# Kernel tuning notes

Measured on AMD Instinct MI355X. Metric: run time of the kernel, lower is better.

Reference implementation:

```python
import jax, jax.numpy as jnp
import numpy as np
from itertools import permutations

EPS = 1e-14


def setup_inputs() -> dict:
    key = jax.random.key(0)
    k1, k2 = jax.random.split(key)
    B, T, S = 512, 8000, 3
    pred = jax.random.normal(k1, (B, T, S), dtype=jnp.float32)
    targets = (jax.random.uniform(k2, (B, T, S)) < 0.3).astype(jnp.float32)
    mask = jnp.ones((B, T), dtype=jnp.float32)
    return {"pred_frames_out": pred, "targets": targets, "mask": mask}


def _pit_loss(pred, targets, mask):
    # pred, targets: [B, T, S]; mask: [B, T]
    B, T, S = pred.shape
    x = pred[:, :, :, None]        # [B,T,S_pred,1]
    t = targets[:, :, None, :]     # [B,T,1,S_tgt]
    # numerically stable BCE-with-logits (same as nn.BCEWithLogitsLoss)
    bce = jnp.maximum(x, 0.0) - x * t + jnp.log1p(jnp.exp(-jnp.abs(x)))  # [B,T,S,S]
    msum = jnp.sum(mask, axis=1) + EPS                                    # [B]
    # cost[b,i,j] = masked mean over time of BCE(pred_i, target_j)
    cost = jnp.einsum('btij,bt->bij', bce, mask) / msum[:, None, None]    # [B,S,S]
    perms = jnp.asarray(list(permutations(range(S))), dtype=jnp.int32)    # [P,S]
    idx_i = jnp.arange(S)[None, :]                                        # [1,S]
    # perm_loss[b,p] = mean_i cost[b, i, perms[p,i]]
    perm_loss = jnp.mean(cost[:, idx_i, perms], axis=-1)                  # [B,P]
    best_val = jnp.min(perm_loss, axis=1)                                 # [B]
    best_idx = jnp.argmin(perm_loss, axis=1)                              # [B]
    return best_val.mean(), best_idx


def reference(pred_frames_out, targets, mask):
    return _pit_loss(pred_frames_out, targets, mask)
```

## Files before the change

### kernel.cpp

```cpp
#include <hip/hip_runtime.h>
#include <math.h>

#define BB 512
#define TT 8000
#define SS 3
#define CH 4
#define TC (TT/CH)
#define NV (TC/4)
#define NACC 13

__device__ __forceinline__ double waveReduceD(double v) {
    #pragma unroll
    for (int o = 32; o > 0; o >>= 1) v += __shfl_down(v, o, 64);
    return v;
}

__global__ __launch_bounds__(256) void pit_partial(
        const float* __restrict__ pred,
        const float* __restrict__ tgt,
        const float* __restrict__ mask,
        double* __restrict__ partials) {
    int blk = blockIdx.x;
    int b = blk / CH, c = blk % CH;
    int tbase = c * TC;
    const float* pp = pred + ((size_t)b * TT + tbase) * 3;
    const float* tp = tgt  + ((size_t)b * TT + tbase) * 3;
    const float* mp = mask + (size_t)b * TT + tbase;

    float acc[NACC];
    #pragma unroll
    for (int k = 0; k < NACC; k++) acc[k] = 0.0f;

    for (int item = threadIdx.x; item < NV; item += 256) {
        const float4* p4 = (const float4*)(pp + (size_t)item * 12);
        float4 pa = p4[0], pb = p4[1], pc = p4[2];
        const float4* t4 = (const float4*)(tp + (size_t)item * 12);
        float4 ta = t4[0], tb = t4[1], tc = t4[2];
        float4 mm = *(const float4*)(mp + (size_t)item * 4);

        float px[4][3] = {{pa.x,pa.y,pa.z},{pa.w,pb.x,pb.y},
                          {pb.z,pb.w,pc.x},{pc.y,pc.z,pc.w}};
        float tx[4][3] = {{ta.x,ta.y,ta.z},{ta.w,tb.x,tb.y},
                          {tb.z,tb.w,tc.x},{tc.y,tc.z,tc.w}};
        float mv[4] = {mm.x, mm.y, mm.z, mm.w};

        #pragma unroll
        for (int u = 0; u < 4; u++) {
            float m = mv[u];
            acc[12] += m;
            #pragma unroll
            for (int i = 0; i < 3; i++) {
                float x = px[u][i];
                float sp = fmaxf(x, 0.0f) + __logf(1.0f + __expf(-fabsf(x)));
                acc[i] = fmaf(m, sp, acc[i]);
                float mx = m * x;
                #pragma unroll
                for (int j = 0; j < 3; j++) {
                    acc[3 + i*3 + j] = fmaf(mx, tx[u][j], acc[3 + i*3 + j]);
                }
            }
        }
    }

    __shared__ double sdata[4][NACC];
    int lane = threadIdx.x & 63, wave = threadIdx.x >> 6;
    #pragma unroll
    for (int k = 0; k < NACC; k++) {
        double v = waveReduceD((double)acc[k]);
        if (lane == 0) sdata[wave][k] = v;
    }
    __syncthreads();
    if (threadIdx.x == 0) {
        #pragma unroll
        for (int k = 0; k < NACC; k++) {
            double s = sdata[0][k] + sdata[1][k] + sdata[2][k] + sdata[3][k];
            partials[(size_t)blk * NACC + k] = s;
        }
    }
}

__global__ __launch_bounds__(64) void pit_finalize(
        const double* __restrict__ partials,
        double* __restrict__ bestv,
        float* __restrict__ out) {
    int b = blockIdx.x * 64 + threadIdx.x;
    if (b >= BB) return;
    double acc[NACC];
    #pragma unroll
    for (int k = 0; k < NACC; k++) {
        double s = 0.0;
        for (int c = 0; c < CH; c++)
            s += partials[((size_t)b * CH + c) * NACC + k];
        acc[k] = s;
    }
    double msum = acc[12] + 1e-14;
    double cost[3][3];
    #pragma unroll
    for (int i = 0; i < 3; i++)
        #pragma unroll
        for (int j = 0; j < 3; j++)
            cost[i][j] = (acc[i] - acc[3 + i*3 + j]) / msum;

    const int perms[6][3] = {{0,1,2},{0,2,1},{1,0,2},{1,2,0},{2,0,1},{2,1,0}};
    double best = 1e300; int bidx = 0;
    #pragma unroll
    for (int p = 0; p < 6; p++) {
        double v = (cost[0][perms[p][0]] + cost[1][perms[p][1]] +
                    cost[2][perms[p][2]]) / 3.0;
        if (v < best) { best = v; bidx = p; }
    }
    bestv[b] = best;
    out[1 + b] = (float)bidx;
}

__global__ __launch_bounds__(256) void pit_mean(
        const double* __restrict__ bestv, float* __restrict__ out) {
    __shared__ double sd[4];
    double v = 0.0;
    for (int b = threadIdx.x; b < BB; b += 256) v += bestv[b];
    int lane = threadIdx.x & 63, wave = threadIdx.x >> 6;
    v = waveReduceD(v);
    if (lane == 0) sd[wave] = v;
    __syncthreads();
    if (threadIdx.x == 0) {
        double s = sd[0] + sd[1] + sd[2] + sd[3];
        out[0] = (float)(s / (double)BB);
    }
}

extern "C" void kernel_launch(void* const* d_in, const int* in_sizes, int n_in,
                              void* d_out, int out_size, void* d_ws, size_t ws_size,
                              hipStream_t stream) {
    const float* pred = (const float*)d_in[0];
    const float* tgt  = (const float*)d_in[1];
    const float* mask = (const float*)d_in[2];
    float* out = (float*)d_out;

    double* partials = (double*)d_ws;
    double* bestv    = partials + (size_t)BB * CH * NACC;

    pit_partial<<<BB * CH, 256, 0, stream>>>(pred, tgt, mask, partials);
    pit_finalize<<<(BB + 63) / 64, 64, 0, stream>>>(partials, bestv, out);
    pit_mean<<<1, 256, 0, stream>>>(bestv, out);
}
```

Measured before the change: 34.54 us.

## Stage chunk data into LDS via direct global-to-LDS loads and merge finalize kernels

Each block now uses 1024 threads and stages its entire chunk of pred, targets and mask into LDS with global_load_lds 16-byte direct loads. It then computes each thread's two elements from LDS, with a float wave-reduce and a double cross-wave sum. The goal is to issue all memory traffic up front for maximum memory-level parallelism instead of looping over vector loads. The finalize and mean kernels are fused into a single 512-thread kernel, removing one launch. This trades larger LDS usage (about 56KB per block), which limits occupancy, and float wave reductions that lose some precision relative to double.

```diff
diff --git a/kernel.cpp b/kernel.cpp
--- a/kernel.cpp
+++ b/kernel.cpp
@@ -3,103 +3,121 @@
 
 #define BB 512
 #define TT 8000
-#define SS 3
 #define CH 4
-#define TC (TT/CH)
-#define NV (TC/4)
+#define TC 2000
 #define NACC 13
+#define NW 16
+#define NF4 3500
+#define NINST 55
 
-__device__ __forceinline__ double waveReduceD(double v) {
+__device__ __forceinline__ void accum_elem(float acc[NACC], float m,
+                                           float x0, float x1, float x2,
+                                           float t0, float t1, float t2) {
+    acc[12] += m;
+    float x[3] = {x0, x1, x2};
+    float t[3] = {t0, t1, t2};
     #pragma unroll
-    for (int o = 32; o > 0; o >>= 1) v += __shfl_down(v, o, 64);
-    return v;
+    for (int i = 0; i < 3; i++) {
+        float xi = x[i];
+        float sp = fmaxf(xi, 0.0f) + __logf(1.0f + __expf(-fabsf(xi)));
+        acc[i] = fmaf(m, sp, acc[i]);
+        float mx = m * xi;
+        #pragma unroll
+        for (int j = 0; j < 3; j++)
+            acc[3 + i*3 + j] = fmaf(mx, t[j], acc[3 + i*3 + j]);
+    }
 }
 
-__global__ __launch_bounds__(256) void pit_partial(
+__global__ __launch_bounds__(1024, 8) void pit_stage(
         const float* __restrict__ pred,
         const float* __restrict__ tgt,
         const float* __restrict__ mask,
         double* __restrict__ partials) {
+    __shared__ float lds[NF4 * 4 + 80];
+    __shared__ float red[NW][NACC];
+
     int blk = blockIdx.x;
-    int b = blk / CH, c = blk % CH;
-    int tbase = c * TC;
-    const float* pp = pred + ((size_t)b * TT + tbase) * 3;
-    const float* tp = tgt  + ((size_t)b * TT + tbase) * 3;
-    const float* mp = mask + (size_t)b * TT + tbase;
+    int b = blk >> 2, c = blk & 3;
+    int tid = threadIdx.x, lane = tid & 63, w = tid >> 6;
+    const float* pb = pred + (size_t)b * (TT*3) + c * (TC*3);
+    const float* tb = tgt  + (size_t)b * (TT*3) + c * (TC*3);
+    const float* mb = mask + (size_t)b * TT + c * TC;
+
+    #pragma unroll
+    for (int k = 0; k < 4; k++) {
+        int n = w + NW * k;
+        if (n < NINST) {
+            int q = n * 64 + lane;
+            const float* src;
+            if (q < 1500)       src = pb + 4 * q;
+            else if (q < 3000)  src = tb + 4 * (q - 1500);
+            else { int mq = q - 3000; mq = mq > 499 ? 499 : mq;
+                   src = mb + 4 * mq; }
+            __builtin_amdgcn_global_load_lds(
+                (const __attribute__((address_space(1))) void*)src,
+                (__attribute__((address_space(3))) void*)(lds + n * 256),
+                16, 0, 0);
+        }
+    }
+    asm volatile("s_waitcnt vmcnt(0)" ::: "memory");
+    __syncthreads();
 
     float acc[NACC];
     #pragma unroll
     for (int k = 0; k < NACC; k++) acc[k] = 0.0f;
 
-    for (int item = threadIdx.x; item < NV; item += 256) {
-        const float4* p4 = (const float4*)(pp + (size_t)item * 12);
-        float4 pa = p4[0], pb = p4[1], pc = p4[2];
-        const float4* t4 = (const float4*)(tp + (size_t)item * 12);
-        float4 ta = t4[0], tb = t4[1], tc = t4[2];
-        float4 mm = *(const float4*)(mp + (size_t)item * 4);
-
-        float px[4][3] = {{pa.x,pa.y,pa.z},{pa.w,pb.x,pb.y},
-                          {pb.z,pb.w,pc.x},{pc.y,pc.z,pc.w}};
-        float tx[4][3] = {{ta.x,ta.y,ta.z},{ta.w,tb.x,tb.y},
-                          {tb.z,tb.w,tc.x},{tc.y,tc.z,tc.w}};
-        float mv[4] = {mm.x, mm.y, mm.z, mm.w};
-
-        #pragma unroll
-        for (int u = 0; u < 4; u++) {
-            float m = mv[u];
-            acc[12] += m;
-            #pragma unroll
-            for (int i = 0; i < 3; i++) {
-                float x = px[u][i];
-                float sp = fmaxf(x, 0.0f) + __logf(1.0f + __expf(-fabsf(x)));
-                acc[i] = fmaf(m, sp, acc[i]);
-                float mx = m * x;
-                #pragma unroll
-                for (int j = 0; j < 3; j++) {
-                    acc[3 + i*3 + j] = fmaf(mx, tx[u][j], acc[3 + i*3 + j]);
-                }
-            }
-        }
+    if (tid < 1000) {
+        int e = 2 * tid;
+        const float* xp = lds + 3 * e;
+        const float* tp = lds + 6000 + 3 * e;
+        float m0 = lds[12000 + e], m1 = lds[12000 + e + 1];
+        accum_elem(acc, m0, xp[0], xp[1], xp[2], tp[0], tp[1], tp[2]);
+        accum_elem(acc, m1, xp[3], xp[4], xp[5], tp[3], tp[4], tp[5]);
     }
 
-    __shared__ double sdata[4][NACC];
-    int lane = threadIdx.x & 63, wave = threadIdx.x >> 6;
     #pragma unroll
     for (int k = 0; k < NACC; k++) {
-        double v = waveReduceD((double)acc[k]);
-        if (lane == 0) sdata[wave][k] = v;
+        float v = acc[k];
+        #pragma unroll
+        for (int o = 32; o > 0; o >>= 1) v += __shfl_xor(v, o, 64);
+        acc[k] = v;
+    }
+    if (lane == 0) {
+        #pragma unroll
+        for (int k = 0; k < NACC; k++) red[w][k] = acc[k];
     }
     __syncthreads();
-    if (threadIdx.x == 0) {
+    if (tid == 0) {
         #pragma unroll
         for (int k = 0; k < NACC; k++) {
-            double s = sdata[0][k] + sdata[1][k] + sdata[2][k] + sdata[3][k];
+            double s = 0.0;
+            #pragma unroll
+            for (int i = 0; i < NW; i++) s += (double)red[i][k];
             partials[(size_t)blk * NACC + k] = s;
         }
     }
 }
 
-__global__ __launch_bounds__(64) void pit_finalize(
-        const double* __restrict__ partials,
-        double* __restrict__ bestv,
-        float* __restrict__ out) {
-    int b = blockIdx.x * 64 + threadIdx.x;
-    if (b >= BB) return;
-    double acc[NACC];
+__global__ __launch_bounds__(512) void pit_final(
+        const double* __restrict__ partials, float* __restrict__ out) {
+    __shared__ double sd[8];
+    int b = threadIdx.x;
+    double a[NACC];
     #pragma unroll
     for (int k = 0; k < NACC; k++) {
         double s = 0.0;
+        #pragma unroll
         for (int c = 0; c < CH; c++)
-            s += partials[((size_t)b * CH + c) * NACC + k];
-        acc[k] = s;
+            s += partials[((size_t)(b * CH + c)) * NACC + k];
+        a[k] = s;
     }
-    double msum = acc[12] + 1e-14;
+    double msum = a[12] + 1e-14;
     double cost[3][3];
     #pragma unroll
     for (int i = 0; i < 3; i++)
         #pragma unroll
         for (int j = 0; j < 3; j++)
-            cost[i][j] = (acc[i] - acc[3 + i*3 + j]) / msum;
+            cost[i][j] = (a[i] - a[3 + i*3 + j]) / msum;
 
     const int perms[6][3] = {{0,1,2},{0,2,1},{1,0,2},{1,2,0},{2,0,1},{2,1,0}};
     double best = 1e300; int bidx = 0;
@@ -109,21 +127,18 @@
                     cost[2][perms[p][2]]) / 3.0;
         if (v < best) { best = v; bidx = p; }
     }
-    bestv[b] = best;
     out[1 + b] = (float)bidx;
-}
 
-__global__ __launch_bounds__(256) void pit_mean(
-        const double* __restrict__ bestv, float* __restrict__ out) {
-    __shared__ double sd[4];
-    double v = 0.0;
-    for (int b = threadIdx.x; b < BB; b += 256) v += bestv[b];
-    int lane = threadIdx.x & 63, wave = threadIdx.x >> 6;
-    v = waveReduceD(v);
-    if (lane == 0) sd[wave] = v;
+    double v = best;
+    #pragma unroll
+    for (int o = 32; o > 0; o >>= 1) v += __shfl_down(v, o, 64);
+    int lane = b & 63, w = b >> 6;
+    if (lane == 0) sd[w] = v;
     __syncthreads();
-    if (threadIdx.x == 0) {
-        double s = sd[0] + sd[1] + sd[2] + sd[3];
+    if (b == 0) {
+        double s = 0.0;
+        #pragma unroll
+        for (int i = 0; i < 8; i++) s += sd[i];
         out[0] = (float)(s / (double)BB);
     }
 }
@@ -135,11 +150,8 @@
     const float* tgt  = (const float*)d_in[1];
     const float* mask = (const float*)d_in[2];
     float* out = (float*)d_out;
+    double* partials = (double*)d_ws;
 
-    double* partials = (double*)d_ws;
-    double* bestv    = partials + (size_t)BB * CH * NACC;
-
-    pit_partial<<<BB * CH, 256, 0, stream>>>(pred, tgt, mask, partials);
-    pit_finalize<<<(BB + 63) / 64, 64, 0, stream>>>(partials, bestv, out);
-    pit_mean<<<1, 256, 0, stream>>>(bestv, out);
+    pit_stage<<<BB * CH, 1024, 0, stream>>>(pred, tgt, mask, partials);
+    pit_final<<<1, 512, 0, stream>>>(partials, out);
 }
```

Result: slower. 59.54 us (+72.4%).
